# Performance work log

Measured on AMD Instinct MI355X. Metric: run time of the kernel, lower is better.

Reference implementation:

```python
import jax, jax.numpy as jnp
import numpy as np

B, S, D, H = 2, 2048, 1024, 16
HD = D // H  # 64

def setup_inputs() -> dict:
    key = jax.random.key(0)
    k1, k2, k3 = jax.random.split(key, 3)
    hidden_states = jax.random.normal(k1, (B, S, D), dtype=jnp.float32)
    w_attn = jax.random.normal(k2, (D, 3 * D), dtype=jnp.float32) * 0.02
    w_proj = jax.random.normal(k3, (D, D), dtype=jnp.float32) * 0.02
    return {"hidden_states": hidden_states, "w_attn": w_attn, "w_proj": w_proj}

def reference(hidden_states, w_attn, w_proj):
    b, s, d = hidden_states.shape
    # c_attn: Conv1D (bias is a scalar zero in the source)
    qkv = jnp.einsum('bsd,de->bse', hidden_states, w_attn)  # [B,S,3D]
    q, k, v = jnp.split(qkv, 3, axis=-1)
    def split_heads(t):
        return t.reshape(b, s, H, HD).transpose(0, 2, 1, 3)  # [B,H,S,HD]
    q, k, v = split_heads(q), split_heads(k), split_heads(v)
    # eager attention; scale_attn_weights=True -> divide by sqrt(head_dim)
    scores = jnp.einsum('bhqd,bhkd->bhqk', q, k) / jnp.sqrt(jnp.float32(HD))
    # NOTE: source registers bias buffer as all-ones (True), so the causal
    # torch.where is a no-op -- faithfully no masking is applied.
    probs = jax.nn.softmax(scores, axis=-1)
    attn = jnp.einsum('bhqk,bhkd->bhqd', probs, v)  # [B,H,S,HD]
    attn = attn.transpose(0, 2, 1, 3).reshape(b, s, d)  # merge heads
    out = jnp.einsum('bsd,de->bse', attn, w_proj)  # c_proj (zero bias)
    return out
```

## Files before the change

kernel.cpp:

```cpp
#include <hip/hip_runtime.h>
#include <hip/hip_bf16.h>

typedef __attribute__((ext_vector_type(8))) short bf16x8;
typedef __attribute__((ext_vector_type(4))) short short4v;
typedef __attribute__((ext_vector_type(4))) float f32x4;
typedef __attribute__((ext_vector_type(16))) float f32x16;
typedef __attribute__((ext_vector_type(4))) float float4v;

__device__ __forceinline__ short f2bf(float f) {
    union { float f; unsigned u; } v; v.f = f;
    unsigned r = v.u + 0x7fffu + ((v.u >> 16) & 1u);
    return (short)(r >> 16);
}
__device__ __forceinline__ float bf2f(short s) {
    union { unsigned u; float f; } v;
    v.u = ((unsigned)(unsigned short)s) << 16;
    return v.f;
}

__device__ __forceinline__ void gload16(const short* g, short* lds) {
    __builtin_amdgcn_global_load_lds(
        (const __attribute__((address_space(1))) unsigned*)g,
        (__attribute__((address_space(3))) unsigned*)lds, 16, 0, 0);
}

__global__ __launch_bounds__(256) void cvt_bf16x8(const float* __restrict__ in,
                                                  short* __restrict__ out) {
    int i = (blockIdx.x * 256 + threadIdx.x) * 8;
    float4v a0 = *reinterpret_cast<const float4v*>(&in[i]);
    float4v a1 = *reinterpret_cast<const float4v*>(&in[i + 4]);
    bf16x8 s;
    s[0] = f2bf(a0[0]); s[1] = f2bf(a0[1]); s[2] = f2bf(a0[2]); s[3] = f2bf(a0[3]);
    s[4] = f2bf(a1[0]); s[5] = f2bf(a1[1]); s[6] = f2bf(a1[2]); s[7] = f2bf(a1[3]);
    *reinterpret_cast<bf16x8*>(&out[i]) = s;
}

__global__ __launch_bounds__(256) void tconv(const float* __restrict__ in,
                                             short* __restrict__ out,
                                             int Kdim, int Ndim) {
    __shared__ int Ls[64][65];
    const int t = threadIdx.x;
    const int k0 = blockIdx.y * 64, n0 = blockIdx.x * 64;
    const int kl = t >> 4, n4 = (t & 15) * 4;
#pragma unroll
    for (int it = 0; it < 4; ++it) {
        int k = kl + it * 16;
        float4v v = *reinterpret_cast<const float4v*>(&in[(size_t)(k0 + k) * Ndim + n0 + n4]);
#pragma unroll
        for (int c = 0; c < 4; ++c) Ls[k][n4 + c] = (int)(unsigned short)f2bf(v[c]);
    }
    __syncthreads();
    const int nl0 = t >> 4, kq = (t & 15) * 4;
#pragma unroll
    for (int it = 0; it < 4; ++it) {
        int nl = nl0 + it * 16;
        short4v s;
#pragma unroll
        for (int j = 0; j < 4; ++j) s[j] = (short)Ls[kq + j][nl];
        *reinterpret_cast<short4v*>(&out[(size_t)(n0 + nl) * Kdim + k0 + kq]) = s;
    }
}

__global__ __launch_bounds__(256) void qkv_gemm(const short* __restrict__ Ah,
                                                const short* __restrict__ Wt,
                                                short* __restrict__ Qw,
                                                short* __restrict__ Kw,
                                                short* __restrict__ Vt) {
    __shared__ short As[128 * 64];
    __shared__ short Bs[128 * 64];
    const int tid = threadIdx.x;
    const int l = tid & 63, w = tid >> 6;
    const int g = l >> 4, lr = l & 15;
    const int r8 = l >> 3, sl = l & 7;
    const int xs = (sl ^ r8) * 8;
    const int wm = (w >> 1) * 64, wn = (w & 1) * 64;
    const int m0 = blockIdx.y * 128;
    const int n0 = blockIdx.x * 128;
    f32x4 acc[4][4] = {};
    for (int k0 = 0; k0 < 1024; k0 += 64) {
        const short* Ag = Ah + m0 * 1024 + k0;
        const short* Bg = Wt + n0 * 1024 + k0;
#pragma unroll
        for (int i = 0; i < 4; ++i) {
            int seg = w * 4 + i;
            gload16(Ag + (seg * 8 + r8) * 1024 + xs, &As[seg * 512]);
            gload16(Bg + (seg * 8 + r8) * 1024 + xs, &Bs[seg * 512]);
        }
        __syncthreads();
#pragma unroll
        for (int kk = 0; kk < 2; ++kk) {
            bf16x8 af[4], bfr[4];
#pragma unroll
            for (int mi = 0; mi < 4; ++mi) {
                int row = wm + mi * 16 + lr;
                af[mi] = *reinterpret_cast<const bf16x8*>(&As[row * 64 + (((4 * kk + g) ^ (lr & 7)) * 8)]);
            }
#pragma unroll
            for (int ni = 0; ni < 4; ++ni) {
                int col = wn + ni * 16 + lr;
                bfr[ni] = *reinterpret_cast<const bf16x8*>(&Bs[col * 64 + (((4 * kk + g) ^ (lr & 7)) * 8)]);
            }
#pragma unroll
            for (int mi = 0; mi < 4; ++mi)
#pragma unroll
                for (int ni = 0; ni < 4; ++ni)
                    acc[mi][ni] = __builtin_amdgcn_mfma_f32_16x16x32_bf16(af[mi], bfr[ni], acc[mi][ni], 0, 0, 0);
        }
        __syncthreads();
    }
#pragma unroll
    for (int mi = 0; mi < 4; ++mi) {
        int m = m0 + wm + mi * 16 + g * 4;
        int bb = m >> 11, s0 = m & 2047;
#pragma unroll
        for (int ni = 0; ni < 4; ++ni) {
            int n = n0 + wn + ni * 16 + lr;
            int which = n >> 10, hh = (n >> 6) & 15, d = n & 63;
            if (which == 2) {
                short4v pv;
#pragma unroll
                for (int r = 0; r < 4; ++r) pv[r] = f2bf(acc[mi][ni][r]);
                *reinterpret_cast<short4v*>(&Vt[(((bb * 16 + hh) * 64) + d) * 2048 + s0]) = pv;
            } else {
                short* dst = which ? Kw : Qw;
                float sc = which ? 1.0f : 0.18033688011112042f;
#pragma unroll
                for (int r = 0; r < 4; ++r)
                    dst[((bb * 16 + hh) * 2048 + s0 + r) * 64 + d] = f2bf(acc[mi][ni][r] * sc);
            }
        }
    }
}

__global__ __launch_bounds__(256, 4) void attn6s(const short* __restrict__ Qw,
                                                 const short* __restrict__ Kw,
                                                 const short* __restrict__ Vt,
                                                 short* __restrict__ N0,
                                                 short* __restrict__ N1,
                                                 float* __restrict__ Tot) {
    __shared__ short Ks[2][64 * 64];
    __shared__ short Vs[2][64 * 64];
    const int tid = threadIdx.x;
    const int w = tid >> 6, l = tid & 63;
    const int q = l & 31, hi = l >> 5;
    const int r8 = l >> 3, sl = l & 7;
    const int xs = (sl ^ r8) * 8;
    const int bid = blockIdx.x;
    const int work = (bid & 7) * 128 + (bid >> 3);
    const int head = work >> 5;
    const int qblk = (work & 31) >> 1;
    const int ks = work & 1;
    const int b = head >> 4, h = head & 15;
    const int q0 = qblk * 128 + w * 32;
    const short* Qb = Qw + ((b * 16 + h) * 2048 + q0) * 64;
    const short* Kb = Kw + ((b * 16 + h) * 2048 + ks * 1024) * 64;
    const short* Vb = Vt + ((b * 16 + h) * 64) * 2048 + ks * 1024;

    bf16x8 qb[4];
#pragma unroll
    for (int c = 0; c < 4; ++c)
        qb[c] = *reinterpret_cast<const bf16x8*>(&Qb[q * 64 + c * 16 + hi * 8]);

    f32x16 o0 = {}, o1 = {};
    float psum = 0.f;

#define STAGE_KV(buf, j0)                                                        \
    {                                                                            \
        _Pragma("unroll")                                                        \
        for (int i = 0; i < 2; ++i) {                                            \
            int seg = w * 2 + i;                                                 \
            gload16(Kb + ((j0) + seg * 8 + r8) * 64 + xs, &Ks[buf][seg * 512]);  \
            gload16(Vb + (seg * 8 + r8) * 2048 + (j0) + xs, &Vs[buf][seg * 512]);\
        }                                                                        \
    }

    STAGE_KV(0, 0);
    __syncthreads();
    int cur = 0;

    for (int jt = 0; jt < 16; ++jt) {
        if (jt < 15) STAGE_KV(cur ^ 1, (jt + 1) * 64);

#pragma unroll
        for (int sub = 0; sub < 2; ++sub) {
            f32x16 st = {};
#pragma unroll
            for (int c = 0; c < 4; ++c) {
                bf16x8 ka = *reinterpret_cast<const bf16x8*>(
                    &Ks[cur][(sub * 32 + q) * 64 + (((2 * c + hi) ^ (q & 7)) * 8)]);
                st = __builtin_amdgcn_mfma_f32_32x32x16_bf16(ka, qb[c], st, 0, 0, 0);
            }
            float p[16];
#pragma unroll
            for (int r = 0; r < 16; ++r) p[r] = __builtin_amdgcn_exp2f(st[r]);
            float s01 = (p[0] + p[1]) + (p[2] + p[3]);
            float s23 = (p[4] + p[5]) + (p[6] + p[7]);
            float s45 = (p[8] + p[9]) + (p[10] + p[11]);
            float s67 = (p[12] + p[13]) + (p[14] + p[15]);
            psum += (s01 + s23) + (s45 + s67);
            int pk[4][2];
#pragma unroll
            for (int bq = 0; bq < 4; ++bq) {
                int w0, w1;
                asm("v_cvt_pk_bf16_f32 %0, %1, %2" : "=v"(w0) : "v"(p[4 * bq]), "v"(p[4 * bq + 1]));
                asm("v_cvt_pk_bf16_f32 %0, %1, %2" : "=v"(w1) : "v"(p[4 * bq + 2]), "v"(p[4 * bq + 3]));
                pk[bq][0] = w0; pk[bq][1] = w1;
            }
#pragma unroll
            for (int c2 = 0; c2 < 2; ++c2) {
                int w0 = pk[2 * c2][0], w2 = pk[2 * c2 + 1][0];
                int w1 = pk[2 * c2][1], w3 = pk[2 * c2 + 1][1];
                asm("v_permlane32_swap_b32 %0, %1" : "+v"(w0), "+v"(w2));
                asm("v_permlane32_swap_b32 %0, %1" : "+v"(w1), "+v"(w3));
                union { int wd[4]; bf16x8 v; } pb;
                pb.wd[0] = w0; pb.wd[1] = w1; pb.wd[2] = w2; pb.wd[3] = w3;
#pragma unroll
                for (int dt = 0; dt < 2; ++dt) {
                    bf16x8 va = *reinterpret_cast<const bf16x8*>(
                        &Vs[cur][(dt * 32 + q) * 64 + (((4 * sub + 2 * c2 + hi) ^ (q & 7)) * 8)]);
                    if (dt == 0) o0 = __builtin_amdgcn_mfma_f32_32x32x16_bf16(va, pb.v, o0, 0, 0, 0);
                    else         o1 = __builtin_amdgcn_mfma_f32_32x32x16_bf16(va, pb.v, o1, 0, 0, 0);
                }
            }
        }
        __syncthreads();
        cur ^= 1;
    }
#undef STAGE_KV

    int pa = __float_as_int(psum), pb2 = pa;
    asm("v_permlane32_swap_b32 %0, %1" : "+v"(pa), "+v"(pb2));
    float tot = __int_as_float(pa) + __int_as_float(pb2);
    float inv = 1.f / tot;

    short* Nd = ks ? N1 : N0;
    short* Orow = &Nd[(b * 2048 + q0 + q) * 1024 + h * 64];
#pragma unroll
    for (int r = 0; r < 4; ++r) {
        short4v ov0, ov1;
#pragma unroll
        for (int j = 0; j < 4; ++j) {
            ov0[j] = f2bf(o0[4 * r + j] * inv);
            ov1[j] = f2bf(o1[4 * r + j] * inv);
        }
        *reinterpret_cast<short4v*>(&Orow[8 * r + 4 * hi]) = ov0;
        *reinterpret_cast<short4v*>(&Orow[32 + 8 * r + 4 * hi]) = ov1;
    }
    if (hi == 0)
        Tot[ks * 65536 + (b * 16 + h) * 2048 + q0 + q] = tot;
}

__global__ __launch_bounds__(256) void attn_merge(short* __restrict__ N0,
                                                  const short* __restrict__ N1,
                                                  const float* __restrict__ Tot) {
    int i = (blockIdx.x * 256 + threadIdx.x) * 8;
    int bs = i >> 10, h = (i >> 6) & 15;
    int b = bs >> 11, s = bs & 2047;
    int qi = (b * 16 + h) * 2048 + s;
    float t0 = Tot[qi], t1 = Tot[65536 + qi];
    float inv = 1.f / (t0 + t1);
    float w0 = t0 * inv, w1 = t1 * inv;
    bf16x8 a = *reinterpret_cast<const bf16x8*>(&N0[i]);
    bf16x8 c = *reinterpret_cast<const bf16x8*>(&N1[i]);
    bf16x8 r;
#pragma unroll
    for (int j = 0; j < 8; ++j) r[j] = f2bf(bf2f(a[j]) * w0 + bf2f(c[j]) * w1);
    *reinterpret_cast<bf16x8*>(&N0[i]) = r;
}

__global__ __launch_bounds__(256) void proj_gemm(const short* __restrict__ Ag,
                                                 const short* __restrict__ Wtp,
                                                 float* __restrict__ Out) {
    __shared__ short As[128 * 64];
    __shared__ short Bs[128 * 64];
    const int tid = threadIdx.x;
    const int l = tid & 63, w = tid >> 6;
    const int g = l >> 4, lr = l & 15;
    const int r8 = l >> 3, sl = l & 7;
    const int xs = (sl ^ r8) * 8;
    const int wm = (w >> 1) * 64, wn = (w & 1) * 64;
    const int m0 = blockIdx.y * 128;
    const int n0 = blockIdx.x * 128;
    f32x4 acc[4][4] = {};
    for (int k0 = 0; k0 < 1024; k0 += 64) {
        const short* Ab = Ag + m0 * 1024 + k0;
        const short* Bg = Wtp + n0 * 1024 + k0;
#pragma unroll
        for (int i = 0; i < 4; ++i) {
            int seg = w * 4 + i;
            gload16(Ab + (seg * 8 + r8) * 1024 + xs, &As[seg * 512]);
            gload16(Bg + (seg * 8 + r8) * 1024 + xs, &Bs[seg * 512]);
        }
        __syncthreads();
#pragma unroll
        for (int kk = 0; kk < 2; ++kk) {
            bf16x8 af[4], bfr[4];
#pragma unroll
            for (int mi = 0; mi < 4; ++mi) {
                int row = wm + mi * 16 + lr;
                af[mi] = *reinterpret_cast<const bf16x8*>(&As[row * 64 + (((4 * kk + g) ^ (lr & 7)) * 8)]);
            }
#pragma unroll
            for (int ni = 0; ni < 4; ++ni) {
                int col = wn + ni * 16 + lr;
                bfr[ni] = *reinterpret_cast<const bf16x8*>(&Bs[col * 64 + (((4 * kk + g) ^ (lr & 7)) * 8)]);
            }
#pragma unroll
            for (int mi = 0; mi < 4; ++mi)
#pragma unroll
                for (int ni = 0; ni < 4; ++ni)
                    acc[mi][ni] = __builtin_amdgcn_mfma_f32_16x16x32_bf16(af[mi], bfr[ni], acc[mi][ni], 0, 0, 0);
        }
        __syncthreads();
    }
#pragma unroll
    for (int mi = 0; mi < 4; ++mi) {
#pragma unroll
        for (int ni = 0; ni < 4; ++ni) {
            int n = n0 + wn + ni * 16 + lr;
#pragma unroll
            for (int r = 0; r < 4; ++r) {
                int mm = m0 + wm + mi * 16 + g * 4 + r;
                Out[mm * 1024 + n] = acc[mi][ni][r];
            }
        }
    }
}

extern "C" void kernel_launch(void* const* d_in, const int* in_sizes, int n_in,
                              void* d_out, int out_size, void* d_ws, size_t ws_size,
                              hipStream_t stream) {
    const float* hidden = (const float*)d_in[0];
    const float* w_attn = (const float*)d_in[1];
    const float* w_proj = (const float*)d_in[2];
    float* out = (float*)d_out;

    short* AhN0 = (short*)d_ws;
    short* Qw = AhN0 + 4194304;
    short* Kw = Qw + 4194304;
    short* Vt = Kw + 4194304;
    short* Wta = (short*)d_out;
    float* Tot = (float*)((char*)d_out + 7u * 1024 * 1024);
    short* N1 = (short*)((char*)d_out + 8u * 1024 * 1024);

    cvt_bf16x8<<<dim3(2048), 256, 0, stream>>>(hidden, AhN0);
    tconv<<<dim3(48, 16), 256, 0, stream>>>(w_attn, Wta, 1024, 3072);
    qkv_gemm<<<dim3(24, 32), 256, 0, stream>>>(AhN0, Wta, Qw, Kw, Vt);
    attn6s<<<dim3(1024), 256, 0, stream>>>(Qw, Kw, Vt, AhN0, N1, Tot);
    attn_merge<<<dim3(2048), 256, 0, stream>>>(AhN0, N1, Tot);
    tconv<<<dim3(16, 16), 256, 0, stream>>>(w_proj, Qw, 1024, 1024);
    proj_gemm<<<dim3(8, 32), 256, 0, stream>>>(AhN0, Qw, out);
}
```

Before: 135.0 us.

## Remap GEMM tiles per XCD and transpose Q/K MFMA for vectorized stores

Both GEMMs switch to a 1D grid whose block IDs are mapped so each XCD (block id mod 8) works on a contiguous rectangle of M/N tiles, aiming to improve L2 reuse of A and B panels on the multi-die MI355X. In the QKV GEMM, Q and K tiles swap the MFMA operand order so each lane holds four consecutive head-dim values. Those values are packed with v_cvt_pk_bf16_f32 and written as a single 8-byte store instead of four scattered 2-byte stores. The isV branch adds code-size duplication, and the tile mapping hardcodes the grid shape.

```diff
diff --git a/kernel.cpp b/kernel.cpp
--- a/kernel.cpp
+++ b/kernel.cpp
@@ -74,8 +74,13 @@
     const int r8 = l >> 3, sl = l & 7;
     const int xs = (sl ^ r8) * 8;
     const int wm = (w >> 1) * 64, wn = (w & 1) * 64;
-    const int m0 = blockIdx.y * 128;
-    const int n0 = blockIdx.x * 128;
+    const int bid = blockIdx.x;
+    const int xcd = bid & 7, idx = bid >> 3;
+    const int nt = (xcd & 1) * 12 + idx % 12;
+    const int mt = (xcd >> 1) * 8 + idx / 12;
+    const int m0 = mt * 128;
+    const int n0 = nt * 128;
+    const bool isV = (n0 >= 2048);
     f32x4 acc[4][4] = {};
     for (int k0 = 0; k0 < 1024; k0 += 64) {
         const short* Ag = Ah + m0 * 1024 + k0;
@@ -100,33 +105,57 @@
                 int col = wn + ni * 16 + lr;
                 bfr[ni] = *reinterpret_cast<const bf16x8*>(&Bs[col * 64 + (((4 * kk + g) ^ (lr & 7)) * 8)]);
             }
-#pragma unroll
-            for (int mi = 0; mi < 4; ++mi)
-#pragma unroll
-                for (int ni = 0; ni < 4; ++ni)
-                    acc[mi][ni] = __builtin_amdgcn_mfma_f32_16x16x32_bf16(af[mi], bfr[ni], acc[mi][ni], 0, 0, 0);
-        }
-        __syncthreads();
-    }
-#pragma unroll
-    for (int mi = 0; mi < 4; ++mi) {
-        int m = m0 + wm + mi * 16 + g * 4;
-        int bb = m >> 11, s0 = m & 2047;
-#pragma unroll
-        for (int ni = 0; ni < 4; ++ni) {
-            int n = n0 + wn + ni * 16 + lr;
-            int which = n >> 10, hh = (n >> 6) & 15, d = n & 63;
-            if (which == 2) {
+            if (isV) {
+#pragma unroll
+                for (int mi = 0; mi < 4; ++mi)
+#pragma unroll
+                    for (int ni = 0; ni < 4; ++ni)
+                        acc[mi][ni] = __builtin_amdgcn_mfma_f32_16x16x32_bf16(af[mi], bfr[ni], acc[mi][ni], 0, 0, 0);
+            } else {
+#pragma unroll
+                for (int mi = 0; mi < 4; ++mi)
+#pragma unroll
+                    for (int ni = 0; ni < 4; ++ni)
+                        acc[mi][ni] = __builtin_amdgcn_mfma_f32_16x16x32_bf16(bfr[ni], af[mi], acc[mi][ni], 0, 0, 0);
+            }
+        }
+        __syncthreads();
+    }
+    if (isV) {
+#pragma unroll
+        for (int mi = 0; mi < 4; ++mi) {
+            int m = m0 + wm + mi * 16 + g * 4;
+            int bb = m >> 11, s0 = m & 2047;
+#pragma unroll
+            for (int ni = 0; ni < 4; ++ni) {
+                int n = n0 + wn + ni * 16 + lr;
+                int hh = (n >> 6) & 15, d = n & 63;
                 short4v pv;
 #pragma unroll
                 for (int r = 0; r < 4; ++r) pv[r] = f2bf(acc[mi][ni][r]);
                 *reinterpret_cast<short4v*>(&Vt[(((bb * 16 + hh) * 64) + d) * 2048 + s0]) = pv;
-            } else {
-                short* dst = which ? Kw : Qw;
-                float sc = which ? 1.0f : 0.18033688011112042f;
-#pragma unroll
-                for (int r = 0; r < 4; ++r)
-                    dst[((bb * 16 + hh) * 2048 + s0 + r) * 64 + d] = f2bf(acc[mi][ni][r] * sc);
+            }
+        }
+    } else {
+        const bool isQ = (n0 < 1024);
+        const float sc = isQ ? 0.18033688011112042f : 1.0f;
+        short* dst = isQ ? Qw : Kw;
+#pragma unroll
+        for (int mi = 0; mi < 4; ++mi) {
+            int m = m0 + wm + mi * 16 + lr;
+            int bb = m >> 11, s0 = m & 2047;
+#pragma unroll
+            for (int ni = 0; ni < 4; ++ni) {
+                int n = n0 + wn + ni * 16 + g * 4;
+                int hh = (n >> 6) & 15, d = n & 63;
+                float a0 = acc[mi][ni][0] * sc, a1 = acc[mi][ni][1] * sc;
+                float a2 = acc[mi][ni][2] * sc, a3 = acc[mi][ni][3] * sc;
+                int w0, w1;
+                asm("v_cvt_pk_bf16_f32 %0, %1, %2" : "=v"(w0) : "v"(a0), "v"(a1));
+                asm("v_cvt_pk_bf16_f32 %0, %1, %2" : "=v"(w1) : "v"(a2), "v"(a3));
+                union { int wd[2]; short4v s; } u;
+                u.wd[0] = w0; u.wd[1] = w1;
+                *reinterpret_cast<short4v*>(&dst[((bb * 16 + hh) * 2048 + s0) * 64 + d]) = u.s;
             }
         }
     }
@@ -254,8 +283,9 @@
                                                   const short* __restrict__ N1,
                                                   const float* __restrict__ Tot) {
     int i = (blockIdx.x * 256 + threadIdx.x) * 8;
-    int bs = i >> 10, h = (i >> 6) & 15;
+    int bs = i >> 10;
     int b = bs >> 11, s = bs & 2047;
+    int h = (i >> 6) & 15;
     int qi = (b * 16 + h) * 2048 + s;
     float t0 = Tot[qi], t1 = Tot[65536 + qi];
     float inv = 1.f / (t0 + t1);
@@ -279,8 +309,12 @@
     const int r8 = l >> 3, sl = l & 7;
     const int xs = (sl ^ r8) * 8;
     const int wm = (w >> 1) * 64, wn = (w & 1) * 64;
-    const int m0 = blockIdx.y * 128;
-    const int n0 = blockIdx.x * 128;
+    const int bid = blockIdx.x;
+    const int xcd = bid & 7, idx = bid >> 3;
+    const int nt = (xcd & 1) * 4 + (idx & 3);
+    const int mt = (xcd >> 1) * 8 + (idx >> 2);
+    const int m0 = mt * 128;
+    const int n0 = nt * 128;
     f32x4 acc[4][4] = {};
     for (int k0 = 0; k0 < 1024; k0 += 64) {
         const short* Ab = Ag + m0 * 1024 + k0;
@@ -345,9 +379,9 @@
 
     cvt_bf16x8<<<dim3(2048), 256, 0, stream>>>(hidden, AhN0);
     tconv<<<dim3(48, 16), 256, 0, stream>>>(w_attn, Wta, 1024, 3072);
-    qkv_gemm<<<dim3(24, 32), 256, 0, stream>>>(AhN0, Wta, Qw, Kw, Vt);
+    qkv_gemm<<<dim3(768), 256, 0, stream>>>(AhN0, Wta, Qw, Kw, Vt);
     attn6s<<<dim3(1024), 256, 0, stream>>>(Qw, Kw, Vt, AhN0, N1, Tot);
     attn_merge<<<dim3(2048), 256, 0, stream>>>(AhN0, N1, Tot);
     tconv<<<dim3(16, 16), 256, 0, stream>>>(w_proj, Qw, 1024, 1024);
-    proj_gemm<<<dim3(8, 32), 256, 0, stream>>>(AhN0, Qw, out);
-}
+    proj_gemm<<<dim3(256), 256, 0, stream>>>(AhN0, Qw, out);
+}
```

After: 131.6 us. 2.5% less time.
